# Optimization experiments

Hardware: AMD Instinct MI355X
Metric: run time of the kernel (lower is better)

The kernel has to match this reference:

```python
import jax, jax.numpy as jnp
import numpy as np


def setup_inputs() -> dict:
    key = jax.random.key(0)
    ks = jax.random.split(key, 12)
    B, N, M, C = 2, 20000, 4096, 6
    S, K, J = 2, 25, 64          # scales, grid cells (2*2+1)^2, neighbors per cell
    Cin = C + 2                   # xy coords concatenated to features
    Cout = 64
    xyz = jax.random.normal(ks[0], (B, N, 3), dtype=jnp.float32)
    feature = jax.random.normal(ks[1], (B, N, C), dtype=jnp.float32)
    new_xyz = jax.random.normal(ks[2], (B, M, 3), dtype=jnp.float32)
    idx = jax.random.randint(ks[3], (S, B, M, K, J), 0, N, dtype=jnp.int32)
    weight = jax.random.uniform(ks[4], (S, B, M, K, J), dtype=jnp.float32)
    conv_w = jax.random.normal(ks[5], (Cout, Cin, K), dtype=jnp.float32) * 0.05
    conv_b = jnp.zeros((Cout,), dtype=jnp.float32)
    mlp_w0 = jax.random.normal(ks[6], (128, S * Cout), dtype=jnp.float32) * 0.05
    mlp_b0 = jnp.zeros((128,), dtype=jnp.float32)
    mlp_w1 = jax.random.normal(ks[7], (256, 128), dtype=jnp.float32) * 0.05
    mlp_b1 = jnp.zeros((256,), dtype=jnp.float32)
    return {"xyz": xyz, "feature": feature, "new_xyz": new_xyz, "idx": idx,
            "weight": weight, "conv_w": conv_w, "conv_b": conv_b,
            "mlp_w0": mlp_w0, "mlp_b0": mlp_b0, "mlp_w1": mlp_w1, "mlp_b1": mlp_b1}


def reference(xyz, feature, new_xyz, idx, weight, conv_w, conv_b,
              mlp_w0, mlp_b0, mlp_w1, mlp_b1):
    # xyz_feature = cat(xy, feature): (B, N, Cin)
    xf = jnp.concatenate([xyz[:, :, :2], feature], axis=-1)
    center2 = new_xyz[:, :, :2]  # (B, M, 2); remaining channels of center are zero

    def per_scale(idx_s, w_s):
        # idx_s, w_s: (B, M, K, J). Gather neighbor features then bilinear-weight.
        gathered = jax.vmap(lambda f, i: f[i])(xf, idx_s)     # (B, M, K, J, Cin)
        nf = jnp.einsum('bmkj,bmkjc->bmkc', w_s, gathered)    # (B, M, K, Cin)
        nf = nf.at[..., :2].add(-center2[:, :, None, :])      # subtract center (xy only)
        # conv2d with kernel (1, K) over the neighbor axis + ReLU
        out = jnp.einsum('bmkc,ock->bom', nf, conv_w) + conv_b[None, :, None]
        return jax.nn.relu(out)                                # (B, Cout, M)

    outs = [per_scale(idx[s], weight[s]) for s in range(idx.shape[0])]
    x = jnp.concatenate(outs, axis=1)                          # (B, S*Cout, M)
    # SharedMLP: 1x1 convs with ReLU (bn=False)
    x = jax.nn.relu(jnp.einsum('bcm,oc->bom', x, mlp_w0) + mlp_b0[None, :, None])
    x = jax.nn.relu(jnp.einsum('bcm,oc->bom', x, mlp_w1) + mlp_b1[None, :, None])
    result_feature = jnp.transpose(x, (0, 2, 1))               # (B, M, 256)
    return new_xyz, result_feature
```

## Files before the change

kernel.cpp:

```cpp
#include <hip/hip_runtime.h>
#include <hip/hip_bf16.h>

#define B 2
#define N 20000
#define M 4096
#define S 2
#define K 25
#define J 64
#define KJ (K*J)
#define TC 32

#define CHUNK 10176
#define GPB   64
#define NTH   1024

__global__ __launch_bounds__(256) void prep_kernel(
    const float* __restrict__ xyz, const float* __restrict__ feature,
    const float* __restrict__ new_xyz, const float* __restrict__ conv_w,
    const float* __restrict__ w0, const float* __restrict__ w1,
    __hip_bfloat16* __restrict__ xfh, float* __restrict__ conv_wT,
    float* __restrict__ w0T, float* __restrict__ w1T,
    float* __restrict__ out_newxyz) {
    const int T1 = B * N * 8;
    const int T2 = 208 * 64;
    const int T3 = B * M * 3;
    const int T4 = 128 * 128;
    const int T5 = 128 * 256;
    int e = blockIdx.x * blockDim.x + threadIdx.x;
    if (e < T1) {
        int r = e >> 3, t = e & 7;
        float v = (t < 2) ? xyz[r * 3 + t] : feature[r * 6 + (t - 2)];
        xfh[e] = __float2bfloat16(v);
    } else if (e < T1 + T2) {
        int e2 = e - T1;
        int i = e2 >> 6, o = e2 & 63;
        conv_wT[e2] = (i < 200) ? conv_w[o * 200 + (i & 7) * 25 + (i >> 3)] : 0.f;
    } else if (e < T1 + T2 + T3) {
        int e3 = e - T1 - T2;
        out_newxyz[e3] = new_xyz[e3];
    } else if (e < T1 + T2 + T3 + T4) {
        int e4 = e - T1 - T2 - T3;
        int c = e4 >> 7, o = e4 & 127;
        w0T[e4] = w0[o * 128 + c];
    } else if (e < T1 + T2 + T3 + T4 + T5) {
        int e5 = e - T1 - T2 - T3 - T4;
        int c = e5 >> 8, o = e5 & 255;
        w1T[e5] = w1[o * 128 + c];
    }
}

__global__ __launch_bounds__(NTH) void gather_conv_kernel(
    const int* __restrict__ idx, const float* __restrict__ weight,
    const float* __restrict__ new_xyz, const uint4* __restrict__ xfh,
    const float* __restrict__ conv_wT, const float* __restrict__ conv_b,
    float* __restrict__ xmid) {
    __shared__ uint4 chunk[CHUNK];

    const int tid = threadIdx.x;
    const int g0  = blockIdx.x * GPB;
    const int b   = (g0 >> 12) & (B - 1);
    const uint4* xfb = xfh + (size_t)b * N;

    for (int r = tid; r < CHUNK; r += NTH) chunk[r] = xfb[r];
    __syncthreads();

    const int team = tid >> 6;
    const int lane = tid & 63;
    const float bo = conv_b[lane];

    for (int u = 0; u < GPB / (NTH / 64); ++u) {
        const int g = g0 + team * (GPB / (NTH / 64)) + u;
        const int m = g & (M - 1);
        const int s = g >> 13;
        const float cx = new_xyz[(b * M + m) * 3 + 0];
        const float cy = new_xyz[(b * M + m) * 3 + 1];
        float acc2 = bo;

        #pragma unroll 1
        for (int p = 0; p < 4; ++p) {
            const int myk = p * 8 + (lane >> 3);
            const bool act = (p < 3) || (lane < 8);
            float acc[8] = {0.f,0.f,0.f,0.f,0.f,0.f,0.f,0.f};
            if (act) {
                const size_t base = (size_t)g * KJ + (size_t)myk * J + (lane & 7) * 8;
                const int4   ia = *(const int4*)  (idx + base);
                const int4   ib = *(const int4*)  (idx + base + 4);
                const float4 wa = *(const float4*)(weight + base);
                const float4 wb = *(const float4*)(weight + base + 4);
                const int   ids[8] = {ia.x, ia.y, ia.z, ia.w, ib.x, ib.y, ib.z, ib.w};
                const float wsv[8] = {wa.x, wa.y, wa.z, wa.w, wb.x, wb.y, wb.z, wb.w};

                uint4 rr[8];
                #pragma unroll
                for (int j = 0; j < 8; ++j)
                    if (ids[j] < CHUNK) rr[j] = chunk[ids[j]];
                #pragma unroll
                for (int j = 0; j < 8; ++j)
                    if (ids[j] >= CHUNK) rr[j] = xfb[ids[j]];

                #pragma unroll
                for (int j = 0; j < 8; ++j) {
                    const uint4 r = rr[j];
                    const float w = wsv[j];
                    acc[0] = fmaf(w, __uint_as_float(r.x << 16),         acc[0]);
                    acc[1] = fmaf(w, __uint_as_float(r.x & 0xffff0000u), acc[1]);
                    acc[2] = fmaf(w, __uint_as_float(r.y << 16),         acc[2]);
                    acc[3] = fmaf(w, __uint_as_float(r.y & 0xffff0000u), acc[3]);
                    acc[4] = fmaf(w, __uint_as_float(r.z << 16),         acc[4]);
                    acc[5] = fmaf(w, __uint_as_float(r.z & 0xffff0000u), acc[5]);
                    acc[6] = fmaf(w, __uint_as_float(r.w << 16),         acc[6]);
                    acc[7] = fmaf(w, __uint_as_float(r.w & 0xffff0000u), acc[7]);
                }
                #pragma unroll
                for (int d = 1; d < 8; d <<= 1) {
                    #pragma unroll
                    for (int c = 0; c < 8; ++c) acc[c] += __shfl_xor(acc[c], d, 64);
                }
                if ((lane & 7) == 0) { acc[0] -= cx; acc[1] -= cy; }
            }
            const int nk = (p < 3) ? 8 : 1;
            #pragma unroll
            for (int kk = 0; kk < 8; ++kk) {
                if (kk < nk) {
                    const float* wrow = conv_wT + (size_t)((p * 8 + kk) * 8) * 64 + lane;
                    #pragma unroll
                    for (int c = 0; c < 8; ++c) {
                        const float v = __shfl(acc[c], kk * 8, 64);
                        acc2 = fmaf(v, wrow[c * 64], acc2);
                    }
                }
            }
        }
        xmid[((size_t)(b * M + m)) * 128 + s * 64 + lane] = fmaxf(acc2, 0.f);
    }
}

__global__ __launch_bounds__(256) void mlp0_kernel(
    float* __restrict__ xmid,
    const float* __restrict__ w0T, const float* __restrict__ b0) {
    __shared__ float ws[128 * 128];
    __shared__ float xs[128 * 32];

    int tid = threadIdx.x;
    int col0 = blockIdx.x * TC;

    {
        const float4* w4 = (const float4*)w0T;
        float4* ws4 = (float4*)ws;
        #pragma unroll
        for (int i = 0; i < 16; ++i) ws4[tid + 256 * i] = w4[tid + 256 * i];
    }
    {
        const float4* xm4 = (const float4*)(xmid + (size_t)col0 * 128);
        #pragma unroll
        for (int r = tid; r < 1024; r += 256) {
            int lc = r >> 5, c4 = r & 31;
            float4 v = xm4[lc * 32 + c4];
            int c = c4 * 4;
            xs[(c + 0) * 32 + lc] = v.x;
            xs[(c + 1) * 32 + lc] = v.y;
            xs[(c + 2) * 32 + lc] = v.z;
            xs[(c + 3) * 32 + lc] = v.w;
        }
    }
    __syncthreads();

    int og = tid >> 3, cg = tid & 7;
    int o0 = og * 4, lc0 = cg * 4;
    float acc[4][4];
    #pragma unroll
    for (int i = 0; i < 4; ++i) {
        float bv = b0[o0 + i];
        #pragma unroll
        for (int u = 0; u < 4; ++u) acc[i][u] = bv;
    }
    for (int c = 0; c < 128; ++c) {
        float4 xv = *(const float4*)&xs[c * 32 + lc0];
        float4 wv = *(const float4*)&ws[c * 128 + o0];
        acc[0][0] = fmaf(wv.x, xv.x, acc[0][0]);
        acc[0][1] = fmaf(wv.x, xv.y, acc[0][1]);
        acc[0][2] = fmaf(wv.x, xv.z, acc[0][2]);
        acc[0][3] = fmaf(wv.x, xv.w, acc[0][3]);
        acc[1][0] = fmaf(wv.y, xv.x, acc[1][0]);
        acc[1][1] = fmaf(wv.y, xv.y, acc[1][1]);
        acc[1][2] = fmaf(wv.y, xv.z, acc[1][2]);
        acc[1][3] = fmaf(wv.y, xv.w, acc[1][3]);
        acc[2][0] = fmaf(wv.z, xv.x, acc[2][0]);
        acc[2][1] = fmaf(wv.z, xv.y, acc[2][1]);
        acc[2][2] = fmaf(wv.z, xv.z, acc[2][2]);
        acc[2][3] = fmaf(wv.z, xv.w, acc[2][3]);
        acc[3][0] = fmaf(wv.w, xv.x, acc[3][0]);
        acc[3][1] = fmaf(wv.w, xv.y, acc[3][1]);
        acc[3][2] = fmaf(wv.w, xv.z, acc[3][2]);
        acc[3][3] = fmaf(wv.w, xv.w, acc[3][3]);
    }
    #pragma unroll
    for (int u = 0; u < 4; ++u) {
        float4 v = make_float4(fmaxf(acc[0][u], 0.f), fmaxf(acc[1][u], 0.f),
                               fmaxf(acc[2][u], 0.f), fmaxf(acc[3][u], 0.f));
        *(float4*)&xmid[(size_t)(col0 + lc0 + u) * 128 + o0] = v;
    }
}

__global__ __launch_bounds__(256) void mlp1_kernel(
    const float* __restrict__ xmid,
    const float* __restrict__ w1T, const float* __restrict__ b1,
    float* __restrict__ out_rf) {
    __shared__ float ws[128 * 128];
    __shared__ float xs[128 * 32];

    int tid = threadIdx.x;
    int bx = blockIdx.x;
    int col0 = (bx >> 1) * TC;
    int oH = (bx & 1) * 128;

    {
        for (int i = tid; i < 4096; i += 256) {
            int c = i >> 5, q = i & 31;
            *(float4*)&ws[c * 128 + q * 4] = *(const float4*)&w1T[c * 256 + oH + q * 4];
        }
    }
    {
        const float4* xm4 = (const float4*)(xmid + (size_t)col0 * 128);
        #pragma unroll
        for (int r = tid; r < 1024; r += 256) {
            int lc = r >> 5, c4 = r & 31;
            float4 v = xm4[lc * 32 + c4];
            int c = c4 * 4;
            xs[(c + 0) * 32 + lc] = v.x;
            xs[(c + 1) * 32 + lc] = v.y;
            xs[(c + 2) * 32 + lc] = v.z;
            xs[(c + 3) * 32 + lc] = v.w;
        }
    }
    __syncthreads();

    int og = tid >> 3, cg = tid & 7;
    int o0 = og * 4, lc0 = cg * 4;
    float acc[4][4];
    #pragma unroll
    for (int i = 0; i < 4; ++i) {
        float bv = b1[oH + o0 + i];
        #pragma unroll
        for (int u = 0; u < 4; ++u) acc[i][u] = bv;
    }
    for (int c = 0; c < 128; ++c) {
        float4 xv = *(const float4*)&xs[c * 32 + lc0];
        float4 wv = *(const float4*)&ws[c * 128 + o0];
        acc[0][0] = fmaf(wv.x, xv.x, acc[0][0]);
        acc[0][1] = fmaf(wv.x, xv.y, acc[0][1]);
        acc[0][2] = fmaf(wv.x, xv.z, acc[0][2]);
        acc[0][3] = fmaf(wv.x, xv.w, acc[0][3]);
        acc[1][0] = fmaf(wv.y, xv.x, acc[1][0]);
        acc[1][1] = fmaf(wv.y, xv.y, acc[1][1]);
        acc[1][2] = fmaf(wv.y, xv.z, acc[1][2]);
        acc[1][3] = fmaf(wv.y, xv.w, acc[1][3]);
        acc[2][0] = fmaf(wv.z, xv.x, acc[2][0]);
        acc[2][1] = fmaf(wv.z, xv.y, acc[2][1]);
        acc[2][2] = fmaf(wv.z, xv.z, acc[2][2]);
        acc[2][3] = fmaf(wv.z, xv.w, acc[2][3]);
        acc[3][0] = fmaf(wv.w, xv.x, acc[3][0]);
        acc[3][1] = fmaf(wv.w, xv.y, acc[3][1]);
        acc[3][2] = fmaf(wv.w, xv.z, acc[3][2]);
        acc[3][3] = fmaf(wv.w, xv.w, acc[3][3]);
    }
    #pragma unroll
    for (int u = 0; u < 4; ++u) {
        float4 v = make_float4(fmaxf(acc[0][u], 0.f), fmaxf(acc[1][u], 0.f),
                               fmaxf(acc[2][u], 0.f), fmaxf(acc[3][u], 0.f));
        *(float4*)&out_rf[(size_t)(col0 + lc0 + u) * 256 + oH + o0] = v;
    }
}

extern "C" void kernel_launch(void* const* d_in, const int* in_sizes, int n_in,
                              void* d_out, int out_size, void* d_ws, size_t ws_size,
                              hipStream_t stream) {
    const float* xyz     = (const float*)d_in[0];
    const float* feature = (const float*)d_in[1];
    const float* new_xyz = (const float*)d_in[2];
    const int*   idx     = (const int*)  d_in[3];
    const float* weight  = (const float*)d_in[4];
    const float* conv_w  = (const float*)d_in[5];
    const float* conv_b  = (const float*)d_in[6];
    const float* mlp_w0  = (const float*)d_in[7];
    const float* mlp_b0  = (const float*)d_in[8];
    const float* mlp_w1  = (const float*)d_in[9];
    const float* mlp_b1  = (const float*)d_in[10];

    float* out    = (float*)d_out;
    float* out_rf = out + (size_t)B * M * 3;

    float* wsf = (float*)d_ws;
    __hip_bfloat16* xfh = (__hip_bfloat16*)wsf;
    float* conv_wT = wsf + 160000;
    float* xmid    = conv_wT + 13312;
    float* w0T     = xmid + 1048576;
    float* w1T     = w0T + 16384;

    {
        int total = 320000 + 13312 + 24576 + 16384 + 32768;
        int blocks = (total + 255) / 256;
        prep_kernel<<<blocks, 256, 0, stream>>>(xyz, feature, new_xyz, conv_w,
                                                mlp_w0, mlp_w1,
                                                xfh, conv_wT, w0T, w1T, out);
    }
    {
        int blocks = (S * B * M) / GPB;
        gather_conv_kernel<<<blocks, NTH, 0, stream>>>(idx, weight, new_xyz,
                                                       (const uint4*)xfh,
                                                       conv_wT, conv_b, xmid);
    }
    {
        mlp0_kernel<<<(B * M) / TC, 256, 0, stream>>>(xmid, w0T, mlp_b0);
    }
    {
        mlp1_kernel<<<2 * (B * M) / TC, 256, 0, stream>>>(xmid, w1T, mlp_b1, out_rf);
    }
}
```

Baseline: 347.3 us.

## Use nontemporal idx/weight loads, batched asm gathers, and float4 conv weights

Streams idx and weight with nontemporal loads so they do not pollute the cache. Replaces the predicated global gathers with eight unconditional inline-asm global loads, clamped to index CHUNK, issued together behind a single waitcnt. Reorders conv_wT into float4-packed layout so each lane reads the conv weights as two float4 loads. This raises memory-level parallelism but adds redundant loads for in-LDS indices and forces a full wait, which blocks the compiler from overlapping those loads with other work.

```diff
diff --git a/kernel.cpp b/kernel.cpp
--- a/kernel.cpp
+++ b/kernel.cpp
@@ -13,6 +13,9 @@
 #define CHUNK 10176
 #define GPB   64
 #define NTH   1024
+
+typedef int   iv4 __attribute__((ext_vector_type(4)));
+typedef float fv4 __attribute__((ext_vector_type(4)));
 
 __global__ __launch_bounds__(256) void prep_kernel(
     const float* __restrict__ xyz, const float* __restrict__ feature,
@@ -33,7 +36,10 @@
         xfh[e] = __float2bfloat16(v);
     } else if (e < T1 + T2) {
         int e2 = e - T1;
-        int i = e2 >> 6, o = e2 & 63;
+        int i4 = e2 >> 8;
+        int rem = e2 & 255;
+        int o = rem >> 2, t = rem & 3;
+        int i = i4 * 4 + t;
         conv_wT[e2] = (i < 200) ? conv_w[o * 200 + (i & 7) * 25 + (i >> 3)] : 0.f;
     } else if (e < T1 + T2 + T3) {
         int e3 = e - T1 - T2;
@@ -67,6 +73,7 @@
     const int team = tid >> 6;
     const int lane = tid & 63;
     const float bo = conv_b[lane];
+    const float4* cw4 = (const float4*)conv_wT;
 
     for (int u = 0; u < GPB / (NTH / 64); ++u) {
         const int g = g0 + team * (GPB / (NTH / 64)) + u;
@@ -80,54 +87,106 @@
         for (int p = 0; p < 4; ++p) {
             const int myk = p * 8 + (lane >> 3);
             const bool act = (p < 3) || (lane < 8);
-            float acc[8] = {0.f,0.f,0.f,0.f,0.f,0.f,0.f,0.f};
+            int   ids[8];
+            float wsv[8];
             if (act) {
                 const size_t base = (size_t)g * KJ + (size_t)myk * J + (lane & 7) * 8;
-                const int4   ia = *(const int4*)  (idx + base);
-                const int4   ib = *(const int4*)  (idx + base + 4);
-                const float4 wa = *(const float4*)(weight + base);
-                const float4 wb = *(const float4*)(weight + base + 4);
-                const int   ids[8] = {ia.x, ia.y, ia.z, ia.w, ib.x, ib.y, ib.z, ib.w};
-                const float wsv[8] = {wa.x, wa.y, wa.z, wa.w, wb.x, wb.y, wb.z, wb.w};
-
-                uint4 rr[8];
+                const iv4 ia = __builtin_nontemporal_load((const iv4*)(idx + base));
+                const iv4 ib = __builtin_nontemporal_load((const iv4*)(idx + base) + 1);
+                const fv4 wa = __builtin_nontemporal_load((const fv4*)(weight + base));
+                const fv4 wb = __builtin_nontemporal_load((const fv4*)(weight + base) + 1);
+                ids[0] = ia.x; ids[1] = ia.y; ids[2] = ia.z; ids[3] = ia.w;
+                ids[4] = ib.x; ids[5] = ib.y; ids[6] = ib.z; ids[7] = ib.w;
+                wsv[0] = wa.x; wsv[1] = wa.y; wsv[2] = wa.z; wsv[3] = wa.w;
+                wsv[4] = wb.x; wsv[5] = wb.y; wsv[6] = wb.z; wsv[7] = wb.w;
+            } else {
                 #pragma unroll
-                for (int j = 0; j < 8; ++j)
-                    if (ids[j] < CHUNK) rr[j] = chunk[ids[j]];
+                for (int j = 0; j < 8; ++j) { ids[j] = CHUNK; wsv[j] = 0.f; }
+            }
+
+            uint4 rr[8];
+            #pragma unroll
+            for (int j = 0; j < 8; ++j)
+                if (ids[j] < CHUNK) rr[j] = chunk[ids[j]];
+
+            {
+                const int ic0 = (ids[0] > CHUNK) ? ids[0] : CHUNK;
+                const int ic1 = (ids[1] > CHUNK) ? ids[1] : CHUNK;
+                const int ic2 = (ids[2] > CHUNK) ? ids[2] : CHUNK;
+                const int ic3 = (ids[3] > CHUNK) ? ids[3] : CHUNK;
+                const int ic4 = (ids[4] > CHUNK) ? ids[4] : CHUNK;
+                const int ic5 = (ids[5] > CHUNK) ? ids[5] : CHUNK;
+                const int ic6 = (ids[6] > CHUNK) ? ids[6] : CHUNK;
+                const int ic7 = (ids[7] > CHUNK) ? ids[7] : CHUNK;
+                const uint4* a0 = xfb + ic0;
+                const uint4* a1 = xfb + ic1;
+                const uint4* a2 = xfb + ic2;
+                const uint4* a3 = xfb + ic3;
+                const uint4* a4 = xfb + ic4;
+                const uint4* a5 = xfb + ic5;
+                const uint4* a6 = xfb + ic6;
+                const uint4* a7 = xfb + ic7;
+                uint4 r0, r1, r2, r3, r4, r5, r6, r7;
+                asm volatile(
+                    "global_load_dwordx4 %0, %8, off sc0\n\t"
+                    "global_load_dwordx4 %1, %9, off sc0\n\t"
+                    "global_load_dwordx4 %2, %10, off sc0\n\t"
+                    "global_load_dwordx4 %3, %11, off sc0\n\t"
+                    "global_load_dwordx4 %4, %12, off sc0\n\t"
+                    "global_load_dwordx4 %5, %13, off sc0\n\t"
+                    "global_load_dwordx4 %6, %14, off sc0\n\t"
+                    "global_load_dwordx4 %7, %15, off sc0\n\t"
+                    "s_waitcnt vmcnt(0)"
+                    : "=&v"(r0), "=&v"(r1), "=&v"(r2), "=&v"(r3),
+                      "=&v"(r4), "=&v"(r5), "=&v"(r6), "=&v"(r7)
+                    : "v"(a0), "v"(a1), "v"(a2), "v"(a3),
+                      "v"(a4), "v"(a5), "v"(a6), "v"(a7));
+                if (ids[0] >= CHUNK) rr[0] = r0;
+                if (ids[1] >= CHUNK) rr[1] = r1;
+                if (ids[2] >= CHUNK) rr[2] = r2;
+                if (ids[3] >= CHUNK) rr[3] = r3;
+                if (ids[4] >= CHUNK) rr[4] = r4;
+                if (ids[5] >= CHUNK) rr[5] = r5;
+                if (ids[6] >= CHUNK) rr[6] = r6;
+                if (ids[7] >= CHUNK) rr[7] = r7;
+            }
+
+            float acc[8] = {0.f,0.f,0.f,0.f,0.f,0.f,0.f,0.f};
+            #pragma unroll
+            for (int j = 0; j < 8; ++j) {
+                const uint4 r = rr[j];
+                const float w = wsv[j];
+                acc[0] = fmaf(w, __uint_as_float(r.x << 16),         acc[0]);
+                acc[1] = fmaf(w, __uint_as_float(r.x & 0xffff0000u), acc[1]);
+                acc[2] = fmaf(w, __uint_as_float(r.y << 16),         acc[2]);
+                acc[3] = fmaf(w, __uint_as_float(r.y & 0xffff0000u), acc[3]);
+                acc[4] = fmaf(w, __uint_as_float(r.z << 16),         acc[4]);
+                acc[5] = fmaf(w, __uint_as_float(r.z & 0xffff0000u), acc[5]);
+                acc[6] = fmaf(w, __uint_as_float(r.w << 16),         acc[6]);
+                acc[7] = fmaf(w, __uint_as_float(r.w & 0xffff0000u), acc[7]);
+            }
+            #pragma unroll
+            for (int d = 1; d < 8; d <<= 1) {
                 #pragma unroll
-                for (int j = 0; j < 8; ++j)
-                    if (ids[j] >= CHUNK) rr[j] = xfb[ids[j]];
-
-                #pragma unroll
-                for (int j = 0; j < 8; ++j) {
-                    const uint4 r = rr[j];
-                    const float w = wsv[j];
-                    acc[0] = fmaf(w, __uint_as_float(r.x << 16),         acc[0]);
-                    acc[1] = fmaf(w, __uint_as_float(r.x & 0xffff0000u), acc[1]);
-                    acc[2] = fmaf(w, __uint_as_float(r.y << 16),         acc[2]);
-                    acc[3] = fmaf(w, __uint_as_float(r.y & 0xffff0000u), acc[3]);
-                    acc[4] = fmaf(w, __uint_as_float(r.z << 16),         acc[4]);
-                    acc[5] = fmaf(w, __uint_as_float(r.z & 0xffff0000u), acc[5]);
-                    acc[6] = fmaf(w, __uint_as_float(r.w << 16),         acc[6]);
-                    acc[7] = fmaf(w, __uint_as_float(r.w & 0xffff0000u), acc[7]);
-                }
-                #pragma unroll
-                for (int d = 1; d < 8; d <<= 1) {
-                    #pragma unroll
-                    for (int c = 0; c < 8; ++c) acc[c] += __shfl_xor(acc[c], d, 64);
-                }
-                if ((lane & 7) == 0) { acc[0] -= cx; acc[1] -= cy; }
-            }
+                for (int c = 0; c < 8; ++c) acc[c] += __shfl_xor(acc[c], d, 64);
+            }
+            if ((lane & 7) == 0) { acc[0] -= cx; acc[1] -= cy; }
+
             const int nk = (p < 3) ? 8 : 1;
             #pragma unroll
             for (int kk = 0; kk < 8; ++kk) {
                 if (kk < nk) {
-                    const float* wrow = conv_wT + (size_t)((p * 8 + kk) * 8) * 64 + lane;
-                    #pragma unroll
-                    for (int c = 0; c < 8; ++c) {
-                        const float v = __shfl(acc[c], kk * 8, 64);
-                        acc2 = fmaf(v, wrow[c * 64], acc2);
-                    }
+                    const int k2 = (p * 8 + kk) * 2;
+                    const float4 w4a = cw4[(k2 + 0) * 64 + lane];
+                    const float4 w4b = cw4[(k2 + 1) * 64 + lane];
+                    acc2 = fmaf(w4a.x, __shfl(acc[0], kk * 8, 64), acc2);
+                    acc2 = fmaf(w4a.y, __shfl(acc[1], kk * 8, 64), acc2);
+                    acc2 = fmaf(w4a.z, __shfl(acc[2], kk * 8, 64), acc2);
+                    acc2 = fmaf(w4a.w, __shfl(acc[3], kk * 8, 64), acc2);
+                    acc2 = fmaf(w4b.x, __shfl(acc[4], kk * 8, 64), acc2);
+                    acc2 = fmaf(w4b.y, __shfl(acc[5], kk * 8, 64), acc2);
+                    acc2 = fmaf(w4b.z, __shfl(acc[6], kk * 8, 64), acc2);
+                    acc2 = fmaf(w4b.w, __shfl(acc[7], kk * 8, 64), acc2);
                 }
             }
         }
```

Result: no change. 345.4 us (-0.6%).

## Two-phase LDS staging of features with multi-center conv and DPP reductions

Applied to the files above, without the earlier changes.

The gather kernel now stages the whole per-batch feature table into LDS in two phases instead of using one chunk plus global fallback loads. Each team processes four centers together so conv weights are read once as float4 and reused, and the 8-lane reductions use DPP instead of shuffles. The center subtraction is moved out of the loop algebraically via precomputed per-channel weight sums, and idx/weight are read with nontemporal loads. The cost is reading idx/weight twice (once per phase), an extra barrier, and masking half the gathers each phase.

```diff
diff --git a/kernel.cpp b/kernel.cpp
--- a/kernel.cpp
+++ b/kernel.cpp
@@ -10,9 +10,18 @@
 #define KJ (K*J)
 #define TC 32
 
-#define CHUNK 10176
+#define C1    10176
 #define GPB   64
 #define NTH   1024
+
+typedef int   iv4 __attribute__((ext_vector_type(4)));
+typedef float fv4 __attribute__((ext_vector_type(4)));
+
+template<int CTRL>
+__device__ __forceinline__ float dppadd(float x) {
+    return x + __int_as_float(
+        __builtin_amdgcn_update_dpp(0, __float_as_int(x), CTRL, 0xF, 0xF, true));
+}
 
 __global__ __launch_bounds__(256) void prep_kernel(
     const float* __restrict__ xyz, const float* __restrict__ feature,
@@ -20,12 +29,13 @@
     const float* __restrict__ w0, const float* __restrict__ w1,
     __hip_bfloat16* __restrict__ xfh, float* __restrict__ conv_wT,
     float* __restrict__ w0T, float* __restrict__ w1T,
-    float* __restrict__ out_newxyz) {
+    float* __restrict__ wsum, float* __restrict__ out_newxyz) {
     const int T1 = B * N * 8;
     const int T2 = 208 * 64;
     const int T3 = B * M * 3;
     const int T4 = 128 * 128;
     const int T5 = 128 * 256;
+    const int T6 = 128;
     int e = blockIdx.x * blockDim.x + threadIdx.x;
     if (e < T1) {
         int r = e >> 3, t = e & 7;
@@ -33,7 +43,10 @@
         xfh[e] = __float2bfloat16(v);
     } else if (e < T1 + T2) {
         int e2 = e - T1;
-        int i = e2 >> 6, o = e2 & 63;
+        int i4 = e2 >> 8;
+        int rem = e2 & 255;
+        int o = rem >> 2, t = rem & 3;
+        int i = i4 * 4 + t;
         conv_wT[e2] = (i < 200) ? conv_w[o * 200 + (i & 7) * 25 + (i >> 3)] : 0.f;
     } else if (e < T1 + T2 + T3) {
         int e3 = e - T1 - T2;
@@ -46,62 +59,74 @@
         int e5 = e - T1 - T2 - T3 - T4;
         int c = e5 >> 8, o = e5 & 255;
         w1T[e5] = w1[o * 128 + c];
-    }
-}
-
-__global__ __launch_bounds__(NTH) void gather_conv_kernel(
+    } else if (e < T1 + T2 + T3 + T4 + T5 + T6) {
+        int e6 = e - T1 - T2 - T3 - T4 - T5;
+        int o = e6 & 63, sel = e6 >> 6;
+        float s = 0.f;
+        for (int k = 0; k < 25; ++k) s += conv_w[o * 200 + sel * 25 + k];
+        wsum[e6] = s;
+    }
+}
+
+__global__ __launch_bounds__(NTH, 4) void gather_conv_kernel(
     const int* __restrict__ idx, const float* __restrict__ weight,
     const float* __restrict__ new_xyz, const uint4* __restrict__ xfh,
     const float* __restrict__ conv_wT, const float* __restrict__ conv_b,
-    float* __restrict__ xmid) {
-    __shared__ uint4 chunk[CHUNK];
+    const float* __restrict__ wsum, float* __restrict__ xmid) {
+    __shared__ uint4 chunk[C1];
 
     const int tid = threadIdx.x;
     const int g0  = blockIdx.x * GPB;
     const int b   = (g0 >> 12) & (B - 1);
     const uint4* xfb = xfh + (size_t)b * N;
 
-    for (int r = tid; r < CHUNK; r += NTH) chunk[r] = xfb[r];
-    __syncthreads();
-
     const int team = tid >> 6;
     const int lane = tid & 63;
-    const float bo = conv_b[lane];
-
-    for (int u = 0; u < GPB / (NTH / 64); ++u) {
-        const int g = g0 + team * (GPB / (NTH / 64)) + u;
-        const int m = g & (M - 1);
-        const int s = g >> 13;
-        const float cx = new_xyz[(b * M + m) * 3 + 0];
-        const float cy = new_xyz[(b * M + m) * 3 + 1];
-        float acc2 = bo;
+    const float4* cw4 = (const float4*)conv_wT;
+
+    float acc2[4] = {0.f, 0.f, 0.f, 0.f};
+
+    #pragma unroll 1
+    for (int ph = 0; ph < 2; ++ph) {
+        const int cbase = ph ? C1 : 0;
+        const int csize = ph ? (N - C1) : C1;
+        if (ph) __syncthreads();
+        for (int r = tid; r < csize; r += NTH) chunk[r] = xfb[cbase + r];
+        __syncthreads();
 
         #pragma unroll 1
         for (int p = 0; p < 4; ++p) {
-            const int myk = p * 8 + (lane >> 3);
+            const int myk  = p * 8 + (lane >> 3);
+            const int mykc = (myk > 24) ? 24 : myk;
             const bool act = (p < 3) || (lane < 8);
-            float acc[8] = {0.f,0.f,0.f,0.f,0.f,0.f,0.f,0.f};
-            if (act) {
-                const size_t base = (size_t)g * KJ + (size_t)myk * J + (lane & 7) * 8;
-                const int4   ia = *(const int4*)  (idx + base);
-                const int4   ib = *(const int4*)  (idx + base + 4);
-                const float4 wa = *(const float4*)(weight + base);
-                const float4 wb = *(const float4*)(weight + base + 4);
+            float ar[4][8];
+
+            #pragma unroll
+            for (int u = 0; u < 4; ++u) {
+                const size_t base = (size_t)(g0 + team * 4 + u) * KJ
+                                  + (size_t)mykc * J + (lane & 7) * 8;
+                const iv4 ia = __builtin_nontemporal_load((const iv4*)(idx + base));
+                const iv4 ib = __builtin_nontemporal_load((const iv4*)(idx + base) + 1);
+                const fv4 wa = __builtin_nontemporal_load((const fv4*)(weight + base));
+                const fv4 wb = __builtin_nontemporal_load((const fv4*)(weight + base) + 1);
                 const int   ids[8] = {ia.x, ia.y, ia.z, ia.w, ib.x, ib.y, ib.z, ib.w};
                 const float wsv[8] = {wa.x, wa.y, wa.z, wa.w, wb.x, wb.y, wb.z, wb.w};
 
                 uint4 rr[8];
+                float we[8];
                 #pragma unroll
-                for (int j = 0; j < 8; ++j)
-                    if (ids[j] < CHUNK) rr[j] = chunk[ids[j]];
-                #pragma unroll
-                for (int j = 0; j < 8; ++j)
-                    if (ids[j] >= CHUNK) rr[j] = xfb[ids[j]];
-
+                for (int j = 0; j < 8; ++j) {
+                    const unsigned rel = (unsigned)(ids[j] - cbase);
+                    const bool inr = (rel < (unsigned)csize) && act;
+                    rr[j] = chunk[inr ? rel : 0u];
+                    we[j] = inr ? wsv[j] : 0.f;
+                }
+
+                float acc[8] = {0.f,0.f,0.f,0.f,0.f,0.f,0.f,0.f};
                 #pragma unroll
                 for (int j = 0; j < 8; ++j) {
                     const uint4 r = rr[j];
-                    const float w = wsv[j];
+                    const float w = we[j];
                     acc[0] = fmaf(w, __uint_as_float(r.x << 16),         acc[0]);
                     acc[1] = fmaf(w, __uint_as_float(r.x & 0xffff0000u), acc[1]);
                     acc[2] = fmaf(w, __uint_as_float(r.y << 16),         acc[2]);
@@ -112,26 +137,49 @@
                     acc[7] = fmaf(w, __uint_as_float(r.w & 0xffff0000u), acc[7]);
                 }
                 #pragma unroll
-                for (int d = 1; d < 8; d <<= 1) {
-                    #pragma unroll
-                    for (int c = 0; c < 8; ++c) acc[c] += __shfl_xor(acc[c], d, 64);
+                for (int c = 0; c < 8; ++c) {
+                    float x = acc[c];
+                    x = dppadd<0xB1>(x);
+                    x = dppadd<0x4E>(x);
+                    x = dppadd<0x141>(x);
+                    ar[u][c] = x;
                 }
-                if ((lane & 7) == 0) { acc[0] -= cx; acc[1] -= cy; }
             }
+
             const int nk = (p < 3) ? 8 : 1;
             #pragma unroll
             for (int kk = 0; kk < 8; ++kk) {
                 if (kk < nk) {
-                    const float* wrow = conv_wT + (size_t)((p * 8 + kk) * 8) * 64 + lane;
+                    const float4 w4a = cw4[(p * 8 + kk) * 128 + lane];
+                    const float4 w4b = cw4[(p * 8 + kk) * 128 + 64 + lane];
                     #pragma unroll
-                    for (int c = 0; c < 8; ++c) {
-                        const float v = __shfl(acc[c], kk * 8, 64);
-                        acc2 = fmaf(v, wrow[c * 64], acc2);
+                    for (int u = 0; u < 4; ++u) {
+                        acc2[u] = fmaf(w4a.x, __shfl(ar[u][0], kk * 8, 64), acc2[u]);
+                        acc2[u] = fmaf(w4a.y, __shfl(ar[u][1], kk * 8, 64), acc2[u]);
+                        acc2[u] = fmaf(w4a.z, __shfl(ar[u][2], kk * 8, 64), acc2[u]);
+                        acc2[u] = fmaf(w4a.w, __shfl(ar[u][3], kk * 8, 64), acc2[u]);
+                        acc2[u] = fmaf(w4b.x, __shfl(ar[u][4], kk * 8, 64), acc2[u]);
+                        acc2[u] = fmaf(w4b.y, __shfl(ar[u][5], kk * 8, 64), acc2[u]);
+                        acc2[u] = fmaf(w4b.z, __shfl(ar[u][6], kk * 8, 64), acc2[u]);
+                        acc2[u] = fmaf(w4b.w, __shfl(ar[u][7], kk * 8, 64), acc2[u]);
                     }
                 }
             }
         }
-        xmid[((size_t)(b * M + m)) * 128 + s * 64 + lane] = fmaxf(acc2, 0.f);
+    }
+
+    const float bo  = conv_b[lane];
+    const float wsx = wsum[lane];
+    const float wsy = wsum[64 + lane];
+    #pragma unroll
+    for (int u = 0; u < 4; ++u) {
+        const int g = g0 + team * 4 + u;
+        const int m = g & (M - 1);
+        const int s = g >> 13;
+        const float cx = new_xyz[(b * M + m) * 3 + 0];
+        const float cy = new_xyz[(b * M + m) * 3 + 1];
+        const float v = acc2[u] + bo - cx * wsx - cy * wsy;
+        xmid[((size_t)(b * M + m)) * 128 + s * 64 + lane] = fmaxf(v, 0.f);
     }
 }
 
@@ -296,19 +344,20 @@
     float* xmid    = conv_wT + 13312;
     float* w0T     = xmid + 1048576;
     float* w1T     = w0T + 16384;
-
-    {
-        int total = 320000 + 13312 + 24576 + 16384 + 32768;
+    float* wsum    = w1T + 32768;
+
+    {
+        int total = 320000 + 13312 + 24576 + 16384 + 32768 + 128;
         int blocks = (total + 255) / 256;
         prep_kernel<<<blocks, 256, 0, stream>>>(xyz, feature, new_xyz, conv_w,
                                                 mlp_w0, mlp_w1,
-                                                xfh, conv_wT, w0T, w1T, out);
+                                                xfh, conv_wT, w0T, w1T, wsum, out);
     }
     {
         int blocks = (S * B * M) / GPB;
         gather_conv_kernel<<<blocks, NTH, 0, stream>>>(idx, weight, new_xyz,
                                                        (const uint4*)xfh,
-                                                       conv_wT, conv_b, xmid);
+                                                       conv_wT, conv_b, wsum, xmid);
     }
     {
         mlp0_kernel<<<(B * M) / TC, 256, 0, stream>>>(xmid, w0T, mlp_b0);
```

Result: no change. 345.9 us (-0.4%).
